# Optimization experiments

Measured on AMD Instinct MI355X. Metric: run time of the kernel, lower is better.

Reference implementation:

```python
import jax, jax.numpy as jnp
import numpy as np

B, L, D, E, H, FFN_MULT = 16, 2048, 512, 8, 8, 4
HD = D // H
ALPHA, BETA, LN_EPS = 1.0, 0.5, 1e-5


def _ln(x, g, b):
    mu = x.mean(-1, keepdims=True)
    var = ((x - mu) ** 2).mean(-1, keepdims=True)
    return (x - mu) * jax.lax.rsqrt(var + LN_EPS) * g + b


def setup_inputs() -> dict:
    key = jax.random.key(0)
    ks = jax.random.split(key, 20)
    s = 0.02
    return {
        "query": jax.random.normal(ks[0], (B, D), jnp.float32),
        "retrieved": jax.random.normal(ks[1], (B, L, D), jnp.float32),
        "w_gate": jax.random.normal(ks[2], (D, E), jnp.float32) * s,
        "ln_q_g": jnp.ones((E, D), jnp.float32),
        "ln_q_b": jnp.zeros((E, D), jnp.float32),
        "Wq": jax.random.normal(ks[3], (E, D, D), jnp.float32) * s,
        "bq": jnp.zeros((E, D), jnp.float32),
        "Wk": jax.random.normal(ks[4], (E, D, D), jnp.float32) * s,
        "bk": jnp.zeros((E, D), jnp.float32),
        "Wv": jax.random.normal(ks[5], (E, D, D), jnp.float32) * s,
        "bv": jnp.zeros((E, D), jnp.float32),
        "Wo": jax.random.normal(ks[6], (E, D, D), jnp.float32) * s,
        "bo": jnp.zeros((E, D), jnp.float32),
        "ln_o_g": jnp.ones((E, D), jnp.float32),
        "ln_o_b": jnp.zeros((E, D), jnp.float32),
        "W1": jax.random.normal(ks[7], (E, D, FFN_MULT * D), jnp.float32) * s,
        "b1": jnp.zeros((E, FFN_MULT * D), jnp.float32),
        "W2": jax.random.normal(ks[8], (E, FFN_MULT * D, D), jnp.float32) * s,
        "b2": jnpp_zeros((E, D)) if False else jnp.zeros((E, D), jnp.float32),
    }


def reference(query, retrieved, w_gate, ln_q_g, ln_q_b, Wq, bq, Wk, bk, Wv, bv,
              Wo, bo, ln_o_g, ln_o_b, W1, b1, W2, b2):
    # Gating (eval mode: no noise, r=None) -> (B, E)
    gates = jax.nn.softmax(query @ w_gate, axis=-1)

    # Per-expert LayerNorm of the (shared) query: normalize once, affine per expert
    mu = query.mean(-1, keepdims=True)
    var = ((query - mu) ** 2).mean(-1, keepdims=True)
    xn = (query - mu) * jax.lax.rsqrt(var + LN_EPS)              # (B, D)
    qn = xn[:, None, :] * ln_q_g[None] + ln_q_b[None]            # (B, E, D)

    # Cross-attention, query length 1, per expert (MHA with in/out proj)
    qh = (jnp.einsum('bed,edk->bek', qn, Wq) + bq).reshape(B, E, H, HD)
    k = (jnp.einsum('bld,edk->belk', retrieved, Wk) + bk[:, None, :]).reshape(B, E, L, H, HD)
    v = (jnp.einsum('bld,edk->belk', retrieved, Wv) + bv[:, None, :]).reshape(B, E, L, H, HD)
    scores = jnp.einsum('behc,belhc->behl', qh, k) / jnp.sqrt(jnp.float32(HD))
    probs = jax.nn.softmax(scores, axis=-1)                      # (B, E, H, L)
    attn = jnp.einsum('behl,belhc->behc', probs, v).reshape(B, E, D)
    attn_out = jnp.einsum('bed,edk->bek', attn, Wo) + bo         # (B, E, D)
    avg_probs = probs.mean(axis=2)                               # (B, E, L) heads averaged

    # Residual + FFN (dropouts inactive at eval)
    x = query[:, None, :] + attn_out                             # (B, E, D)
    xo = _ln(x, ln_o_g[None], ln_o_b[None])
    h = jax.nn.gelu(jnp.einsum('bed,edf->bef', xo, W1) + b1, approximate=False)
    y = jnp.einsum('bef,efd->bed', h, W2) + b2 + x               # expert_outs (B, E, D)

    # Entropy-derived reliability
    p = jnp.clip(avg_probs, 1e-12, None)
    Hent = -(p * jnp.log(p)).sum(-1)                             # (B, E)
    s_all = jnp.exp(-BETA * Hent)

    gt = gates * s_all
    gt = gt / (gt.sum(-1, keepdims=True) + 1e-9)
    mixture = (gt[..., None] * y).sum(1)                         # (B, D)
    fused = ALPHA * mixture + (1.0 - ALPHA) * query
    return fused, y, gt
```

## Files before the change

### kernel.cpp

```cpp
#include <hip/hip_runtime.h>
#include <math.h>

#define CB 16
#define CL 2048
#define CD 512
#define CE 8
#define CH 8
#define CEH 64
#define CF 2048

typedef __bf16 bf16x8 __attribute__((ext_vector_type(8)));
typedef float f32x4 __attribute__((ext_vector_type(4)));

#define GLL16(srcp, dstp) __builtin_amdgcn_global_load_lds( \
    (const __attribute__((address_space(1))) unsigned int*)(srcp), \
    (__attribute__((address_space(3))) unsigned int*)(dstp), 16, 0, 0)

#define WS_GATES 0
#define WS_XN    (WS_GATES + CB*CE)
#define WS_QN    (WS_XN + CB*CD)
#define WS_QH    (WS_QN + CB*CE*CD)
#define WS_SBIAS (WS_QH + CB*CE*CD)
#define WS_WK    (WS_SBIAS + CB*CE*CH)
#define WS_SC    (WS_WK + CB*CEH*CD)
#define WS_PART  WS_SC
#define WS_PART1 (WS_PART + 524288)
#define WS_RMAX  (WS_SC + CB*CL*CEH)
#define WS_RINV  (WS_RMAX + CB*CEH)
#define WS_ENT   (WS_RINV + CB*CEH)
#define WS_ATTN  (WS_ENT + CB*CE*8)
#define WS_X     (WS_ATTN + CB*CE*CD)
#define WS_XO    (WS_X + CB*CE*CD)
#define WS_HB    (WS_XO + CB*CE*CD)
#define WS_RP    (WS_HB + CB*CE*CF)
#define WS_PB16  (WS_RP + 8*CB*CEH*CD)

__global__ __launch_bounds__(256) void k1_gates_qn(
    const float* __restrict__ q, const float* __restrict__ wg,
    const float* __restrict__ g, const float* __restrict__ bln,
    float* __restrict__ qn, float* __restrict__ gates) {
  int b = blockIdx.x, t = threadIdx.x;
  __shared__ float red[256];
  __shared__ float logits[CE];
  float v0 = q[b*CD + t], v1 = q[b*CD + 256 + t];
  red[t] = v0 + v1; __syncthreads();
  for (int s = 128; s > 0; s >>= 1) { if (t < s) red[t] += red[t+s]; __syncthreads(); }
  float mu = red[0] * (1.0f/CD); __syncthreads();
  float c0 = v0 - mu, c1 = v1 - mu;
  red[t] = c0*c0 + c1*c1; __syncthreads();
  for (int s = 128; s > 0; s >>= 1) { if (t < s) red[t] += red[t+s]; __syncthreads(); }
  float rstd = rsqrtf(red[0] * (1.0f/CD) + 1e-5f); __syncthreads();
  float xn0 = c0 * rstd, xn1 = c1 * rstd;
  #pragma unroll
  for (int e = 0; e < CE; e++) {
    qn[(b*CE + e)*CD + t]       = xn0 * g[e*CD + t]       + bln[e*CD + t];
    qn[(b*CE + e)*CD + 256 + t] = xn1 * g[e*CD + 256 + t] + bln[e*CD + 256 + t];
  }
  float ge[CE];
  #pragma unroll
  for (int e = 0; e < CE; e++) ge[e] = v0 * wg[t*CE + e] + v1 * wg[(256+t)*CE + e];
  for (int e = 0; e < CE; e++) {
    red[t] = ge[e]; __syncthreads();
    for (int s = 128; s > 0; s >>= 1) { if (t < s) red[t] += red[t+s]; __syncthreads(); }
    if (t == 0) logits[e] = red[0];
    __syncthreads();
  }
  if (t == 0) {
    float m = logits[0];
    for (int e = 1; e < CE; e++) m = fmaxf(m, logits[e]);
    float s = 0.f, ex[CE];
    for (int e = 0; e < CE; e++) { ex[e] = __expf(logits[e] - m); s += ex[e]; }
    for (int e = 0; e < CE; e++) gates[b*CE + e] = ex[e] / s;
  }
}

template<int KC>
__global__ __launch_bounds__(256) void gstream(
    const float* __restrict__ X, int xb_, int xe_,
    const float* __restrict__ W, size_t we_, int ldw,
    float* __restrict__ P, int ntiles, size_t pc_, int pb_, int pe_) {
  int e = blockIdx.y;
  int nt = blockIdx.x % ntiles, kc = blockIdx.x / ntiles;
  int n0 = nt * 64, k0 = kc * KC;
  __shared__ float xs[KC][16];
  __shared__ float red[16][64];
  int t = threadIdx.x;
  for (int idx = t; idx < KC * 16; idx += 256) {
    int k = idx >> 4, b = idx & 15;
    xs[k][b] = X[(size_t)b * xb_ + (size_t)e * xe_ + k0 + k];
  }
  __syncthreads();
  int n = t & 63, kq = t >> 6;
  float acc[16] = {};
  const float* Wp = W + (size_t)e * we_ + (size_t)k0 * ldw + n0 + n;
  #pragma unroll 4
  for (int k = kq * (KC/4); k < (kq+1) * (KC/4); k++) {
    float w = Wp[(size_t)k * ldw];
    const float4* xp = reinterpret_cast<const float4*>(xs[k]);
    float4 x0 = xp[0], x1 = xp[1], x2 = xp[2], x3 = xp[3];
    acc[0]  += x0.x*w; acc[1]  += x0.y*w; acc[2]  += x0.z*w; acc[3]  += x0.w*w;
    acc[4]  += x1.x*w; acc[5]  += x1.y*w; acc[6]  += x1.z*w; acc[7]  += x1.w*w;
    acc[8]  += x2.x*w; acc[9]  += x2.y*w; acc[10] += x2.z*w; acc[11] += x2.w*w;
    acc[12] += x3.x*w; acc[13] += x3.y*w; acc[14] += x3.z*w; acc[15] += x3.w*w;
  }
  if (kq == 0) {
    #pragma unroll
    for (int b = 0; b < 16; b++) red[b][n] = acc[b];
  }
  __syncthreads();
  #pragma unroll
  for (int qq = 1; qq < 4; qq++) {
    if (kq == qq) {
      #pragma unroll
      for (int b = 0; b < 16; b++) red[b][n] += acc[b];
    }
    __syncthreads();
  }
  #pragma unroll
  for (int i = 0; i < 4; i++) {
    int b = kq*4 + i;
    P[(size_t)kc*pc_ + (size_t)b*pb_ + (size_t)e*pe_ + n0 + n] = red[b][n];
  }
}

__global__ __launch_bounds__(256) void gstream_v(
    const float* __restrict__ rp, const float* __restrict__ Wv,
    float* __restrict__ P) {
  int eh = blockIdx.y, kc = blockIdx.x;
  int e = eh >> 3, h = eh & 7;
  int k0 = kc * 64;
  __shared__ float xs[64][20];
  __shared__ float red[16][64];
  int t = threadIdx.x;
  for (int idx = t; idx < 64 * 16; idx += 256) {
    int k = idx & 63, b = idx >> 6;
    float s = 0.f;
    #pragma unroll
    for (int c = 0; c < 8; c++)
      s += rp[(size_t)c*(CB*CEH*CD) + ((size_t)(b*CEH + eh))*CD + k0 + k];
    xs[k][b] = s;
  }
  __syncthreads();
  int n = t & 63, kq = t >> 6;
  float acc[16] = {};
  const float* Wp = Wv + (size_t)e*CD*CD + (size_t)k0*CD + h*64 + n;
  #pragma unroll 4
  for (int k = kq*16; k < kq*16 + 16; k++) {
    float w = Wp[(size_t)k * CD];
    const float4* xp = reinterpret_cast<const float4*>(&xs[k][0]);
    float4 x0 = xp[0], x1 = xp[1], x2 = xp[2], x3 = xp[3];
    acc[0]  += x0.x*w; acc[1]  += x0.y*w; acc[2]  += x0.z*w; acc[3]  += x0.w*w;
    acc[4]  += x1.x*w; acc[5]  += x1.y*w; acc[6]  += x1.z*w; acc[7]  += x1.w*w;
    acc[8]  += x2.x*w; acc[9]  += x2.y*w; acc[10] += x2.z*w; acc[11] += x2.w*w;
    acc[12] += x3.x*w; acc[13] += x3.y*w; acc[14] += x3.z*w; acc[15] += x3.w*w;
  }
  if (kq == 0) { 
    #pragma unroll
    for (int b = 0; b < 16; b++) red[b][n] = acc[b]; }
  __syncthreads();
  #pragma unroll
  for (int qq = 1; qq < 4; qq++) {
    if (kq == qq) {
      #pragma unroll
      for (int b = 0; b < 16; b++) red[b][n] += acc[b];
    }
    __syncthreads();
  }
  #pragma unroll
  for (int i = 0; i < 4; i++) {
    int b = kq*4 + i;
    P[(size_t)kc*65536 + (size_t)b*4096 + (size_t)eh*64 + n] = red[b][n];
  }
}

__global__ __launch_bounds__(256) void gstream_wo(
    const float* __restrict__ Pv, const float* __restrict__ bv,
    const float* __restrict__ Wo, float* __restrict__ P) {
  int e = blockIdx.y;
  int nt = blockIdx.x % 8, kc = blockIdx.x / 8;
  int n0 = nt * 64, k0 = kc * 64;
  __shared__ float xs[64][20];
  __shared__ float red[16][64];
  int t = threadIdx.x;
  for (int idx = t; idx < 64 * 16; idx += 256) {
    int k = idx & 63, b = idx >> 6;
    float s = bv[e*CD + k0 + k];
    #pragma unroll
    for (int c = 0; c < 8; c++)
      s += Pv[(size_t)c*65536 + (size_t)b*4096 + e*512 + k0 + k];
    xs[k][b] = s;
  }
  __syncthreads();
  int n = t & 63, kq = t >> 6;
  float acc[16] = {};
  const float* Wp = Wo + (size_t)e*CD*CD + (size_t)k0*CD + n0 + n;
  #pragma unroll 4
  for (int k = kq*16; k < kq*16 + 16; k++) {
    float w = Wp[(size_t)k * CD];
    const float4* xp = reinterpret_cast<const float4*>(&xs[k][0]);
    float4 x0 = xp[0], x1 = xp[1], x2 = xp[2], x3 = xp[3];
    acc[0]  += x0.x*w; acc[1]  += x0.y*w; acc[2]  += x0.z*w; acc[3]  += x0.w*w;
    acc[4]  += x1.x*w; acc[5]  += x1.y*w; acc[6]  += x1.z*w; acc[7]  += x1.w*w;
    acc[8]  += x2.x*w; acc[9]  += x2.y*w; acc[10] += x2.z*w; acc[11] += x2.w*w;
    acc[12] += x3.x*w; acc[13] += x3.y*w; acc[14] += x3.z*w; acc[15] += x3.w*w;
  }
  if (kq == 0) {
    #pragma unroll
    for (int b = 0; b < 16; b++) red[b][n] = acc[b]; }
  __syncthreads();
  #pragma unroll
  for (int qq = 1; qq < 4; qq++) {
    if (kq == qq) {
      #pragma unroll
      for (int b = 0; b < 16; b++) red[b][n] += acc[b];
    }
    __syncthreads();
  }
  #pragma unroll
  for (int i = 0; i < 4; i++) {
    int b = kq*4 + i;
    P[(size_t)kc*65536 + (size_t)b*4096 + (size_t)e*512 + n0 + n] = red[b][n];
  }
}

__global__ __launch_bounds__(512) void comb_qh_sbias(
    const float* __restrict__ P, const float* __restrict__ bq,
    const float* __restrict__ bk, float* __restrict__ qh,
    float* __restrict__ sbias) {
  int be = blockIdx.x, b = be >> 3, e = be & 7, t = threadIdx.x;
  float s = bq[e*CD + t];
  #pragma unroll
  for (int c = 0; c < 8; c++)
    s += P[(size_t)c*65536 + (size_t)b*4096 + e*512 + t];
  qh[be*CD + t] = s;
  float w = s * bk[e*CD + t];
  #pragma unroll
  for (int off = 32; off > 0; off >>= 1) w += __shfl_down(w, off);
  if ((t & 63) == 0) sbias[be*CH + (t >> 6)] = w;
}

__global__ __launch_bounds__(512) void comb_o_lno(
    const float* __restrict__ P, const float* __restrict__ bo,
    const float* __restrict__ q, const float* __restrict__ g,
    const float* __restrict__ bb, float* __restrict__ xb,
    float* __restrict__ xo) {
  int be = blockIdx.x, b = be >> 3, e = be & 7, t = threadIdx.x;
  float v = q[b*CD + t] + bo[e*CD + t];
  #pragma unroll
  for (int c = 0; c < 8; c++)
    v += P[(size_t)c*65536 + (size_t)b*4096 + e*512 + t];
  xb[be*CD + t] = v;
  __shared__ float red[512];
  red[t] = v; __syncthreads();
  for (int s = 256; s > 0; s >>= 1) { if (t < s) red[t] += red[t+s]; __syncthreads(); }
  float mu = red[0] * (1.0f/CD); __syncthreads();
  float c0 = v - mu;
  red[t] = c0*c0; __syncthreads();
  for (int s = 256; s > 0; s >>= 1) { if (t < s) red[t] += red[t+s]; __syncthreads(); }
  float rstd = rsqrtf(red[0] * (1.0f/CD) + 1e-5f);
  xo[be*CD + t] = c0*rstd*g[e*CD + t] + bb[e*CD + t];
}

__global__ __launch_bounds__(256) void comb4_gelu(
    const float* __restrict__ P, const float* __restrict__ bias,
    float* __restrict__ out) {
  int i = blockIdx.x*256 + threadIdx.x;
  float s = bias[i & 16383];
  #pragma unroll
  for (int c = 0; c < 4; c++) s += P[(size_t)c*262144 + i];
  out[i] = 0.5f*s*(1.f + erff(s*0.70710678118f));
}

__global__ __launch_bounds__(512) void comb_ffn2_final(
    const float* __restrict__ P, const float* __restrict__ b2,
    const float* __restrict__ xb, const float* __restrict__ gates,
    const float* __restrict__ entp, float* __restrict__ yout,
    float* __restrict__ fused, float* __restrict__ gtout) {
  int b = blockIdx.x, t = threadIdx.x;
  __shared__ float gt_s[CE];
  if (t < CE) {
    float Hs = 0.f;
    #pragma unroll
    for (int c = 0; c < 8; c++) Hs += entp[(b*CE + t)*8 + c];
    gt_s[t] = gates[b*CE + t] * __expf(-0.5f * Hs);
  }
  __syncthreads();
  if (t == 0) {
    float s = 0.f;
    for (int e = 0; e < CE; e++) s += gt_s[e];
    s += 1e-9f;
    for (int e = 0; e < CE; e++) gt_s[e] /= s;
  }
  __syncthreads();
  float acc = 0.f;
  #pragma unroll
  for (int e = 0; e < CE; e++) {
    float y = b2[e*CD + t] + xb[(b*CE + e)*CD + t];
    #pragma unroll
    for (int c = 0; c < 8; c++)
      y += P[(size_t)c*65536 + (size_t)b*4096 + e*512 + t];
    yout[(b*CE + e)*CD + t] = y;
    acc += gt_s[e] * y;
  }
  fused[b*CD + t] = acc;
  if (t < CE) gtout[b*CE + t] = gt_s[t];
}

__global__ __launch_bounds__(256) void k4_wkeff(
    const float* __restrict__ Wk, const float* __restrict__ qh,
    __bf16* __restrict__ wkh) {
  int e = blockIdx.y;
  int h = blockIdx.x >> 3, dt = blockIdx.x & 7;
  int d0 = dt * 64;
  __shared__ float wks[64][65];
  __shared__ float qs[64][16];
  __shared__ float red[16][64];
  int t = threadIdx.x;
  for (int idx = t; idx < 64*64; idx += 256) {
    int c = idx & 63, d = idx >> 6;
    wks[c][d] = Wk[(size_t)e*CD*CD + (size_t)(d0+d)*CD + h*64 + c];
  }
  for (int idx = t; idx < 64*16; idx += 256) {
    int c = idx >> 4, b = idx & 15;
    qs[c][b] = qh[(b*CE + e)*CD + h*64 + c];
  }
  __syncthreads();
  int d = t & 63, cq = t >> 6;
  float acc[16] = {};
  #pragma unroll 4
  for (int c = cq*16; c < cq*16 + 16; c++) {
    float w = wks[c][d];
    const float4* xp = reinterpret_cast<const float4*>(qs[c]);
    float4 x0 = xp[0], x1 = xp[1], x2 = xp[2], x3 = xp[3];
    acc[0]  += x0.x*w; acc[1]  += x0.y*w; acc[2]  += x0.z*w; acc[3]  += x0.w*w;
    acc[4]  += x1.x*w; acc[5]  += x1.y*w; acc[6]  += x1.z*w; acc[7]  += x1.w*w;
    acc[8]  += x2.x*w; acc[9]  += x2.y*w; acc[10] += x2.z*w; acc[11] += x2.w*w;
    acc[12] += x3.x*w; acc[13] += x3.y*w; acc[14] += x3.z*w; acc[15] += x3.w*w;
  }
  if (cq == 0) { 
    #pragma unroll
    for (int b = 0; b < 16; b++) red[b][d] = acc[b]; }
  __syncthreads();
  #pragma unroll
  for (int qq = 1; qq < 4; qq++) {
    if (cq == qq) {
      #pragma unroll
      for (int b = 0; b < 16; b++) red[b][d] += acc[b];
    }
    __syncthreads();
  }
  int eh = e*8 + h;
  #pragma unroll
  for (int i = 0; i < 4; i++) {
    int b = cq*4 + i;
    wkh[((size_t)(b*CEH + eh))*CD + d0 + d] = (__bf16)red[b][d];
  }
}

__global__ __launch_bounds__(256) void k5_mfma(
    const float* __restrict__ ret, const __bf16* __restrict__ wkh,
    const float* __restrict__ sbias, float* __restrict__ sc,
    float* __restrict__ lmax, float* __restrict__ lsum) {
  int b = blockIdx.y, lt = blockIdx.x, t = threadIdx.x;
  int w = t >> 6, lane = t & 63;
  int lnlo = lane & 15, lnhi = lane >> 4;
  int lh = w & 1, ehh = w >> 1;
  int l0blk = lt*32;
  int ehbase = ehh*32;
  __shared__ __align__(16) char ldsbuf[32768];
  f32x4 acc[2];
  acc[0] = (f32x4){0.f,0.f,0.f,0.f};
  acc[1] = (f32x4){0.f,0.f,0.f,0.f};
  const float*  retb  = ret + (size_t)(b*CL + l0blk)*CD;
  const __bf16* wkhb  = wkh + (size_t)b*CEH*CD;

  int rs0 = t,        rl0 = rs0 >> 4, rg0 = ((rs0 & 15) ^ (rl0 & 15)) << 2;
  int rs1 = t + 256,  rl1 = rs1 >> 4, rg1 = ((rs1 & 15) ^ (rl1 & 15)) << 2;
  int ws0 = t,        we0 = ws0 >> 3, wg0 = ((ws0 & 7) ^ (we0 & 7)) << 3;
  int ws1 = t + 256,  we1 = ws1 >> 3, wg1 = ((ws1 & 7) ^ (we1 & 7)) << 3;

  #define K5_STAGE(bufi, kt) do {                                          \
    char* rB = ldsbuf + (bufi)*8192;                                       \
    char* wB = ldsbuf + 16384 + (bufi)*8192;                               \
    int dofs = (kt)*64;                                                    \
    GLL16(retb + (size_t)rl0*CD + dofs + rg0, rB + rs0*16);                \
    GLL16(retb + (size_t)rl1*CD + dofs + rg1, rB + rs1*16);                \
    GLL16(wkhb + (size_t)we0*CD + dofs + wg0, wB + ws0*16);                \
    GLL16(wkhb + (size_t)we1*CD + dofs + wg1, wB + ws1*16);                \
  } while (0)

  K5_STAGE(0, 0);
  __syncthreads();
  #pragma unroll
  for (int kt = 0; kt < 8; kt++) {
    int cur = kt & 1;
    if (kt < 7) K5_STAGE(cur ^ 1, kt + 1);
    const char* rB = ldsbuf + cur*8192;
    const char* wB = ldsbuf + 16384 + cur*8192;
    #pragma unroll
    for (int sub = 0; sub < 2; sub++) {
      int g0 = (sub*8 + lnhi*2 + 0) ^ lnlo;
      int g1 = (sub*8 + lnhi*2 + 1) ^ lnlo;
      float4 f0 = *reinterpret_cast<const float4*>(rB + (lh*16 + lnlo)*256 + g0*16);
      float4 f1 = *reinterpret_cast<const float4*>(rB + (lh*16 + lnlo)*256 + g1*16);
      bf16x8 bfrag;
      bfrag[0]=(__bf16)f0.x; bfrag[1]=(__bf16)f0.y; bfrag[2]=(__bf16)f0.z; bfrag[3]=(__bf16)f0.w;
      bfrag[4]=(__bf16)f1.x; bfrag[5]=(__bf16)f1.y; bfrag[6]=(__bf16)f1.z; bfrag[7]=(__bf16)f1.w;
      int ga = (sub*4 + lnhi) ^ (lnlo & 7);
      bf16x8 a0 = *reinterpret_cast<const bf16x8*>(wB + (ehbase + 0*16 + lnlo)*128 + ga*16);
      bf16x8 a1 = *reinterpret_cast<const bf16x8*>(wB + (ehbase + 1*16 + lnlo)*128 + ga*16);
      acc[0] = __builtin_amdgcn_mfma_f32_16x16x32_bf16(a0, bfrag, acc[0], 0, 0, 0);
      acc[1] = __builtin_amdgcn_mfma_f32_16x16x32_bf16(a1, bfrag, acc[1], 0, 0, 0);
    }
    __syncthreads();
  }
  #undef K5_STAGE

  int strip = lt*2 + lh;
  int l = l0blk + lh*16 + lnlo;
  #pragma unroll
  for (int et = 0; et < 2; et++) {
    #pragma unroll
    for (int i = 0; i < 4; i++) {
      int eh = ehbase + et*16 + lnhi*4 + i;
      float v = acc[et][i]*0.125f + sbias[b*CEH + eh]*0.125f;
      sc[((size_t)(b*CEH + eh))*CL + l] = v;
      float m = v;
      m = fmaxf(m, __shfl_xor(m, 1));
      m = fmaxf(m, __shfl_xor(m, 2));
      m = fmaxf(m, __shfl_xor(m, 4));
      m = fmaxf(m, __shfl_xor(m, 8));
      float s = __expf(v - m);
      s += __shfl_xor(s, 1);
      s += __shfl_xor(s, 2);
      s += __shfl_xor(s, 4);
      s += __shfl_xor(s, 8);
      if (lnlo == et*4 + i) {
        lmax[((size_t)(b*CEH + eh))*128 + strip] = m;
        lsum[((size_t)(b*CEH + eh))*128 + strip] = s;
      }
    }
  }
}

__global__ __launch_bounds__(256) void k5b2(
    const float* __restrict__ lmax, const float* __restrict__ lsum,
    float* __restrict__ rmax, float* __restrict__ rinv) {
  int b = blockIdx.x, t = threadIdx.x, eh = t & 63, q = t >> 6;
  const float* lm = lmax + ((size_t)(b*CEH + eh))*128 + q*32;
  const float* ls = lsum + ((size_t)(b*CEH + eh))*128 + q*32;
  float M = -1e30f, S = 0.f;
  for (int i = 0; i < 32; i++) {
    float m2 = lm[i], s2 = ls[i];
    float Mn = fmaxf(M, m2);
    S = S*__expf(M - Mn) + s2*__expf(m2 - Mn);
    M = Mn;
  }
  __shared__ float sm[4][64], ss[4][64];
  sm[q][eh] = M; ss[q][eh] = S;
  __syncthreads();
  if (q == 0) {
    #pragma unroll
    for (int i = 1; i < 4; i++) {
      float m2 = sm[i][eh], s2 = ss[i][eh];
      float Mn = fmaxf(M, m2);
      S = S*__expf(M - Mn) + s2*__expf(m2 - Mn);
      M = Mn;
    }
    rmax[b*CEH + eh] = M;
    rinv[b*CEH + eh] = 1.f / S;
  }
}

__global__ __launch_bounds__(256) void k5n(
    const float* __restrict__ sc, const float* __restrict__ rmax,
    const float* __restrict__ rinv, __bf16* __restrict__ pb,
    float* __restrict__ entp) {
  int e = blockIdx.x, b = blockIdx.y, lc = blockIdx.z, t = threadIdx.x;
  int l = lc*256 + t;
  float pbav = 0.f;
  #pragma unroll
  for (int h = 0; h < 8; h++) {
    size_t ix = ((size_t)(b*CEH + e*8 + h))*CL + l;
    float p = __expf(sc[ix] - rmax[b*CEH + e*8 + h]) * rinv[b*CEH + e*8 + h];
    pb[ix] = (__bf16)p;
    pbav += p;
  }
  pbav = fmaxf(pbav*0.125f, 1e-12f);
  float ent = -pbav * __logf(pbav);
  __shared__ float red[256];
  red[t] = ent; __syncthreads();
  for (int s = 128; s > 0; s >>= 1) { if (t < s) red[t] += red[t+s]; __syncthreads(); }
  if (t == 0) entp[(b*CE + e)*8 + lc] = red[0];
}

__global__ __launch_bounds__(256) void k6_mfma(
    const __bf16* __restrict__ pb, const float* __restrict__ ret,
    float* __restrict__ part) {
  int b = blockIdx.y;
  int dt = blockIdx.x & 7, lc = blockIdx.x >> 3;
  int d0 = dt*64, l0 = lc*256;
  int t = threadIdx.x, w = t >> 6, lane = t & 63;
  int lnlo = lane & 15, lnhi = lane >> 4;
  __shared__ __bf16 Bs[2][64][40];
  f32x4 acc[4];
  #pragma unroll
  for (int et = 0; et < 4; et++) acc[et] = (f32x4){0.f,0.f,0.f,0.f};
  const __bf16* pbb = pb + ((size_t)(b*CEH) + lnlo)*CL + l0 + lnhi*8;
  int srow = t & 31, scol = (t >> 5)*8;
  const float* retb = ret + ((size_t)(b*CL) + l0 + srow)*CD + d0 + scol;
  float4 v0 = *reinterpret_cast<const float4*>(retb);
  float4 v1 = *reinterpret_cast<const float4*>(retb + 4);
  bf16x8 ap0 = *reinterpret_cast<const bf16x8*>(pbb);
  bf16x8 ap1 = *reinterpret_cast<const bf16x8*>(pbb + (size_t)16*CL);
  bf16x8 ap2 = *reinterpret_cast<const bf16x8*>(pbb + (size_t)32*CL);
  bf16x8 ap3 = *reinterpret_cast<const bf16x8*>(pbb + (size_t)48*CL);
  #pragma unroll
  for (int kt = 0; kt < 8; kt++) {
    int cur = kt & 1;
    Bs[cur][scol+0][srow] = (__bf16)v0.x; Bs[cur][scol+1][srow] = (__bf16)v0.y;
    Bs[cur][scol+2][srow] = (__bf16)v0.z; Bs[cur][scol+3][srow] = (__bf16)v0.w;
    Bs[cur][scol+4][srow] = (__bf16)v1.x; Bs[cur][scol+5][srow] = (__bf16)v1.y;
    Bs[cur][scol+6][srow] = (__bf16)v1.z; Bs[cur][scol+7][srow] = (__bf16)v1.w;
    bf16x8 an0, an1, an2, an3;
    if (kt < 7) {
      v0 = *reinterpret_cast<const float4*>(retb + (size_t)(kt+1)*32*CD);
      v1 = *reinterpret_cast<const float4*>(retb + (size_t)(kt+1)*32*CD + 4);
      an0 = *reinterpret_cast<const bf16x8*>(pbb + (kt+1)*32);
      an1 = *reinterpret_cast<const bf16x8*>(pbb + (size_t)16*CL + (kt+1)*32);
      an2 = *reinterpret_cast<const bf16x8*>(pbb + (size_t)32*CL + (kt+1)*32);
      an3 = *reinterpret_cast<const bf16x8*>(pbb + (size_t)48*CL + (kt+1)*32);
    }
    __syncthreads();
    bf16x8 bfrag = *reinterpret_cast<const bf16x8*>(&Bs[cur][w*16 + lnlo][lnhi*8]);
    acc[0] = __builtin_amdgcn_mfma_f32_16x16x32_bf16(ap0, bfrag, acc[0], 0, 0, 0);
    acc[1] = __builtin_amdgcn_mfma_f32_16x16x32_bf16(ap1, bfrag, acc[1], 0, 0, 0);
    acc[2] = __builtin_amdgcn_mfma_f32_16x16x32_bf16(ap2, bfrag, acc[2], 0, 0, 0);
    acc[3] = __builtin_amdgcn_mfma_f32_16x16x32_bf16(ap3, bfrag, acc[3], 0, 0, 0);
    if (kt < 7) { ap0 = an0; ap1 = an1; ap2 = an2; ap3 = an3; }
  }
  float* dst = part + (size_t)lc*(CB*CEH*CD);
  int d = d0 + w*16 + lnlo;
  #pragma unroll
  for (int et = 0; et < 4; et++) {
    #pragma unroll
    for (int i = 0; i < 4; i++) {
      int eh = et*16 + lnhi*4 + i;
      dst[((size_t)(b*CEH + eh))*CD + d] = acc[et][i];
    }
  }
}

extern "C" void kernel_launch(void* const* d_in, const int* in_sizes, int n_in,
                              void* d_out, int out_size, void* d_ws, size_t ws_size,
                              hipStream_t stream) {
  const float* q    = (const float*)d_in[0];
  const float* ret  = (const float*)d_in[1];
  const float* wg   = (const float*)d_in[2];
  const float* lnqg = (const float*)d_in[3];
  const float* lnqb = (const float*)d_in[4];
  const float* Wq   = (const float*)d_in[5];
  const float* bq   = (const float*)d_in[6];
  const float* Wk   = (const float*)d_in[7];
  const float* bk   = (const float*)d_in[8];
  const float* Wv   = (const float*)d_in[9];
  const float* bv   = (const float*)d_in[10];
  const float* Wo   = (const float*)d_in[11];
  const float* bo   = (const float*)d_in[12];
  const float* lnog = (const float*)d_in[13];
  const float* lnob = (const float*)d_in[14];
  const float* W1   = (const float*)d_in[15];
  const float* b1   = (const float*)d_in[16];
  const float* W2   = (const float*)d_in[17];
  const float* b2   = (const float*)d_in[18];

  float* ws = (float*)d_ws;
  float* fused = (float*)d_out;
  float* yout  = fused + CB*CD;
  float* gtout = yout + CB*CE*CD;

  float* gates = ws + WS_GATES;
  float* qn    = ws + WS_QN;
  float* qh    = ws + WS_QH;
  float* sbias = ws + WS_SBIAS;
  __bf16* wkh  = (__bf16*)(ws + WS_WK);
  float* sc    = ws + WS_SC;
  float* part0 = ws + WS_PART;
  float* part1 = ws + WS_PART1;
  float* rmax  = ws + WS_RMAX;
  float* rinv  = ws + WS_RINV;
  float* entp  = ws + WS_ENT;
  float* xb    = ws + WS_X;
  float* xo    = ws + WS_XO;
  float* hbuf  = ws + WS_HB;
  float* rpart = ws + WS_RP;
  __bf16* pb16 = (__bf16*)(ws + WS_PB16);
  float* lmax  = rpart;
  float* lsum  = rpart + CB*CEH*128;

  k1_gates_qn<<<CB, 256, 0, stream>>>(q, wg, lnqg, lnqb, qn, gates);
  gstream<64><<<dim3(64, CE), 256, 0, stream>>>(qn, CE*CD, CD, Wq, (size_t)CD*CD, CD,
                                                part0, 8, 65536, CE*CD, CD);
  comb_qh_sbias<<<CB*CE, 512, 0, stream>>>(part0, bq, bk, qh, sbias);
  k4_wkeff<<<dim3(64, CE), 256, 0, stream>>>(Wk, qh, wkh);
  k5_mfma<<<dim3(64, CB), 256, 0, stream>>>(ret, wkh, sbias, sc, lmax, lsum);
  k5b2<<<CB, 256, 0, stream>>>(lmax, lsum, rmax, rinv);
  k5n<<<dim3(CE, CB, 8), 256, 0, stream>>>(sc, rmax, rinv, pb16, entp);
  k6_mfma<<<dim3(64, CB), 256, 0, stream>>>(pb16, ret, rpart);
  gstream_v<<<dim3(8, CEH), 256, 0, stream>>>(rpart, Wv, part1);
  gstream_wo<<<dim3(64, CE), 256, 0, stream>>>(part1, bv, Wo, part0);
  comb_o_lno<<<CB*CE, 512, 0, stream>>>(part0, bo, q, lnog, lnob, xb, xo);
  gstream<128><<<dim3(128, CE), 256, 0, stream>>>(xo, CE*CD, CD, W1, (size_t)CD*CF, CF,
                                                  part0, 32, 262144, CE*CF, CF);
  comb4_gelu<<<1024, 256, 0, stream>>>(part0, b1, hbuf);
  gstream<256><<<dim3(64, CE), 256, 0, stream>>>(hbuf, CE*CF, CF, W2, (size_t)CF*CD, CD,
                                                 part0, 8, 65536, CE*CD, CD);
  comb_ffn2_final<<<CB, 512, 0, stream>>>(part0, b2, xb, gates, entp, yout, fused, gtout);
}
```

Before: 129.0 us.

## Fuse combine kernels into consumers and use wave shuffles in gating

Folds three small combine kernels into the kernels that consume their results: the Q-projection partial sum and sbias go into k4_wkeff, the softmax max/sum reduction goes into k5n, and the bias+GELU step goes into a new W2 streaming kernel. This cuts three launches and the round trips through qh, rmax/rinv and hbuf. In exchange the fused kernels recompute the combines redundantly across blocks (for example GELU is recomputed per n-tile, and the lmax/lsum merge per l-chunk). The gating kernel also replaces shared-memory tree reductions with wave shuffles and fewer barriers.

```diff
diff --git a/kernel.cpp b/kernel.cpp
--- a/kernel.cpp
+++ b/kernel.cpp
@@ -25,9 +25,7 @@
 #define WS_SC    (WS_WK + CB*CEH*CD)
 #define WS_PART  WS_SC
 #define WS_PART1 (WS_PART + 524288)
-#define WS_RMAX  (WS_SC + CB*CL*CEH)
-#define WS_RINV  (WS_RMAX + CB*CEH)
-#define WS_ENT   (WS_RINV + CB*CEH)
+#define WS_ENT   (WS_SC + CB*CL*CEH)
 #define WS_ATTN  (WS_ENT + CB*CE*8)
 #define WS_X     (WS_ATTN + CB*CE*CD)
 #define WS_XO    (WS_X + CB*CE*CD)
@@ -40,37 +38,54 @@
     const float* __restrict__ g, const float* __restrict__ bln,
     float* __restrict__ qn, float* __restrict__ gates) {
   int b = blockIdx.x, t = threadIdx.x;
-  __shared__ float red[256];
-  __shared__ float logits[CE];
+  int w = t >> 6, lane = t & 63;
+  __shared__ float r1[4], r2[4];
+  __shared__ float gp[4][8];
   float v0 = q[b*CD + t], v1 = q[b*CD + 256 + t];
-  red[t] = v0 + v1; __syncthreads();
-  for (int s = 128; s > 0; s >>= 1) { if (t < s) red[t] += red[t+s]; __syncthreads(); }
-  float mu = red[0] * (1.0f/CD); __syncthreads();
+  float s = v0 + v1;
+  #pragma unroll
+  for (int m = 32; m >= 1; m >>= 1) s += __shfl_xor(s, m);
+  if (lane == 0) r1[w] = s;
+  __syncthreads();
+  float mu = (r1[0]+r1[1]+r1[2]+r1[3]) * (1.0f/CD);
   float c0 = v0 - mu, c1 = v1 - mu;
-  red[t] = c0*c0 + c1*c1; __syncthreads();
-  for (int s = 128; s > 0; s >>= 1) { if (t < s) red[t] += red[t+s]; __syncthreads(); }
-  float rstd = rsqrtf(red[0] * (1.0f/CD) + 1e-5f); __syncthreads();
+  s = c0*c0 + c1*c1;
+  #pragma unroll
+  for (int m = 32; m >= 1; m >>= 1) s += __shfl_xor(s, m);
+  if (lane == 0) r2[w] = s;
+  float ge[CE];
+  #pragma unroll
+  for (int e = 0; e < CE; e++) ge[e] = v0 * wg[t*CE + e] + v1 * wg[(256+t)*CE + e];
+  #pragma unroll
+  for (int m = 32; m >= 1; m >>= 1) {
+    #pragma unroll
+    for (int e = 0; e < CE; e++) ge[e] += __shfl_xor(ge[e], m);
+  }
+  if (lane == 0) {
+    #pragma unroll
+    for (int e = 0; e < CE; e++) gp[w][e] = ge[e];
+  }
+  __syncthreads();
+  float rstd = rsqrtf((r2[0]+r2[1]+r2[2]+r2[3]) * (1.0f/CD) + 1e-5f);
   float xn0 = c0 * rstd, xn1 = c1 * rstd;
   #pragma unroll
   for (int e = 0; e < CE; e++) {
     qn[(b*CE + e)*CD + t]       = xn0 * g[e*CD + t]       + bln[e*CD + t];
     qn[(b*CE + e)*CD + 256 + t] = xn1 * g[e*CD + 256 + t] + bln[e*CD + 256 + t];
   }
-  float ge[CE];
-  #pragma unroll
-  for (int e = 0; e < CE; e++) ge[e] = v0 * wg[t*CE + e] + v1 * wg[(256+t)*CE + e];
-  for (int e = 0; e < CE; e++) {
-    red[t] = ge[e]; __syncthreads();
-    for (int s = 128; s > 0; s >>= 1) { if (t < s) red[t] += red[t+s]; __syncthreads(); }
-    if (t == 0) logits[e] = red[0];
-    __syncthreads();
-  }
   if (t == 0) {
-    float m = logits[0];
-    for (int e = 1; e < CE; e++) m = fmaxf(m, logits[e]);
-    float s = 0.f, ex[CE];
-    for (int e = 0; e < CE; e++) { ex[e] = __expf(logits[e] - m); s += ex[e]; }
-    for (int e = 0; e < CE; e++) gates[b*CE + e] = ex[e] / s;
+    float logit[CE];
+    float m = -1e30f;
+    #pragma unroll
+    for (int e = 0; e < CE; e++) {
+      logit[e] = gp[0][e] + gp[1][e] + gp[2][e] + gp[3][e];
+      m = fmaxf(m, logit[e]);
+    }
+    float ssum = 0.f, ex[CE];
+    #pragma unroll
+    for (int e = 0; e < CE; e++) { ex[e] = __expf(logit[e] - m); ssum += ex[e]; }
+    #pragma unroll
+    for (int e = 0; e < CE; e++) gates[b*CE + e] = ex[e] / ssum;
   }
 }
 
@@ -223,20 +238,54 @@
   }
 }
 
-__global__ __launch_bounds__(512) void comb_qh_sbias(
-    const float* __restrict__ P, const float* __restrict__ bq,
-    const float* __restrict__ bk, float* __restrict__ qh,
-    float* __restrict__ sbias) {
-  int be = blockIdx.x, b = be >> 3, e = be & 7, t = threadIdx.x;
-  float s = bq[e*CD + t];
-  #pragma unroll
-  for (int c = 0; c < 8; c++)
-    s += P[(size_t)c*65536 + (size_t)b*4096 + e*512 + t];
-  qh[be*CD + t] = s;
-  float w = s * bk[e*CD + t];
-  #pragma unroll
-  for (int off = 32; off > 0; off >>= 1) w += __shfl_down(w, off);
-  if ((t & 63) == 0) sbias[be*CH + (t >> 6)] = w;
+__global__ __launch_bounds__(256) void gstream_w2(
+    const float* __restrict__ P1, const float* __restrict__ b1,
+    const float* __restrict__ W2, float* __restrict__ Pout) {
+  int e = blockIdx.y;
+  int nt = blockIdx.x % 8, kc = blockIdx.x / 8;
+  int n0 = nt * 64, k0 = kc * 256;
+  __shared__ float xs[256][16];
+  __shared__ float red[16][64];
+  int t = threadIdx.x;
+  for (int idx = t; idx < 256 * 16; idx += 256) {
+    int k = idx >> 4, b = idx & 15;
+    float v = b1[e*CF + k0 + k];
+    #pragma unroll
+    for (int c = 0; c < 4; c++)
+      v += P1[(size_t)c*262144 + (size_t)b*16384 + e*2048 + k0 + k];
+    xs[k][b] = 0.5f*v*(1.f + erff(v*0.70710678118f));
+  }
+  __syncthreads();
+  int n = t & 63, kq = t >> 6;
+  float acc[16] = {};
+  const float* Wp = W2 + (size_t)e*CF*CD + (size_t)k0*CD + n0 + n;
+  #pragma unroll 4
+  for (int k = kq*64; k < kq*64 + 64; k++) {
+    float w = Wp[(size_t)k * CD];
+    const float4* xp = reinterpret_cast<const float4*>(xs[k]);
+    float4 x0 = xp[0], x1 = xp[1], x2 = xp[2], x3 = xp[3];
+    acc[0]  += x0.x*w; acc[1]  += x0.y*w; acc[2]  += x0.z*w; acc[3]  += x0.w*w;
+    acc[4]  += x1.x*w; acc[5]  += x1.y*w; acc[6]  += x1.z*w; acc[7]  += x1.w*w;
+    acc[8]  += x2.x*w; acc[9]  += x2.y*w; acc[10] += x2.z*w; acc[11] += x2.w*w;
+    acc[12] += x3.x*w; acc[13] += x3.y*w; acc[14] += x3.z*w; acc[15] += x3.w*w;
+  }
+  if (kq == 0) {
+    #pragma unroll
+    for (int b = 0; b < 16; b++) red[b][n] = acc[b]; }
+  __syncthreads();
+  #pragma unroll
+  for (int qq = 1; qq < 4; qq++) {
+    if (kq == qq) {
+      #pragma unroll
+      for (int b = 0; b < 16; b++) red[b][n] += acc[b];
+    }
+    __syncthreads();
+  }
+  #pragma unroll
+  for (int i = 0; i < 4; i++) {
+    int b = kq*4 + i;
+    Pout[(size_t)kc*65536 + (size_t)b*4096 + (size_t)e*512 + n0 + n] = red[b][n];
+  }
 }
 
 __global__ __launch_bounds__(512) void comb_o_lno(
@@ -261,16 +310,6 @@
   xo[be*CD + t] = c0*rstd*g[e*CD + t] + bb[e*CD + t];
 }
 
-__global__ __launch_bounds__(256) void comb4_gelu(
-    const float* __restrict__ P, const float* __restrict__ bias,
-    float* __restrict__ out) {
-  int i = blockIdx.x*256 + threadIdx.x;
-  float s = bias[i & 16383];
-  #pragma unroll
-  for (int c = 0; c < 4; c++) s += P[(size_t)c*262144 + i];
-  out[i] = 0.5f*s*(1.f + erff(s*0.70710678118f));
-}
-
 __global__ __launch_bounds__(512) void comb_ffn2_final(
     const float* __restrict__ P, const float* __restrict__ b2,
     const float* __restrict__ xb, const float* __restrict__ gates,
@@ -307,8 +346,9 @@
 }
 
 __global__ __launch_bounds__(256) void k4_wkeff(
-    const float* __restrict__ Wk, const float* __restrict__ qh,
-    __bf16* __restrict__ wkh) {
+    const float* __restrict__ Wk, const float* __restrict__ Pq,
+    const float* __restrict__ bq, const float* __restrict__ bk,
+    __bf16* __restrict__ wkh, float* __restrict__ sbias) {
   int e = blockIdx.y;
   int h = blockIdx.x >> 3, dt = blockIdx.x & 7;
   int d0 = dt * 64;
@@ -322,9 +362,25 @@
   }
   for (int idx = t; idx < 64*16; idx += 256) {
     int c = idx >> 4, b = idx & 15;
-    qs[c][b] = qh[(b*CE + e)*CD + h*64 + c];
-  }
-  __syncthreads();
+    float s = bq[e*CD + h*64 + c];
+    #pragma unroll
+    for (int cc = 0; cc < 8; cc++)
+      s += Pq[(size_t)cc*65536 + (size_t)b*4096 + e*512 + h*64 + c];
+    qs[c][b] = s;
+  }
+  __syncthreads();
+  if (dt == 0) {
+    int bb = t >> 4, ii = t & 15;
+    float p = 0.f;
+    #pragma unroll
+    for (int j = 0; j < 4; j++)
+      p += qs[ii*4 + j][bb] * bk[e*CD + h*64 + ii*4 + j];
+    p += __shfl_xor(p, 1);
+    p += __shfl_xor(p, 2);
+    p += __shfl_xor(p, 4);
+    p += __shfl_xor(p, 8);
+    if (ii == 0) sbias[bb*CEH + e*8 + h] = p;
+  }
   int d = t & 63, cq = t >> 6;
   float acc[16] = {};
   #pragma unroll 4
@@ -443,46 +499,41 @@
   }
 }
 
-__global__ __launch_bounds__(256) void k5b2(
-    const float* __restrict__ lmax, const float* __restrict__ lsum,
-    float* __restrict__ rmax, float* __restrict__ rinv) {
-  int b = blockIdx.x, t = threadIdx.x, eh = t & 63, q = t >> 6;
-  const float* lm = lmax + ((size_t)(b*CEH + eh))*128 + q*32;
-  const float* ls = lsum + ((size_t)(b*CEH + eh))*128 + q*32;
-  float M = -1e30f, S = 0.f;
-  for (int i = 0; i < 32; i++) {
-    float m2 = lm[i], s2 = ls[i];
-    float Mn = fmaxf(M, m2);
-    S = S*__expf(M - Mn) + s2*__expf(m2 - Mn);
-    M = Mn;
-  }
-  __shared__ float sm[4][64], ss[4][64];
-  sm[q][eh] = M; ss[q][eh] = S;
-  __syncthreads();
-  if (q == 0) {
-    #pragma unroll
-    for (int i = 1; i < 4; i++) {
-      float m2 = sm[i][eh], s2 = ss[i][eh];
+__global__ __launch_bounds__(256) void k5n(
+    const float* __restrict__ sc, const float* __restrict__ lmax,
+    const float* __restrict__ lsum, __bf16* __restrict__ pb,
+    float* __restrict__ entp) {
+  int e = blockIdx.x, b = blockIdx.y, lc = blockIdx.z, t = threadIdx.x;
+  __shared__ float M_s[8], I_s[8];
+  {
+    int g = t >> 5, lane = t & 31;
+    int eh = e*8 + g;
+    const float* lm = lmax + ((size_t)(b*CEH + eh))*128;
+    const float* ls = lsum + ((size_t)(b*CEH + eh))*128;
+    float M = -1e30f, S = 0.f;
+    #pragma unroll
+    for (int j = 0; j < 4; j++) {
+      float m2 = lm[lane + j*32], s2 = ls[lane + j*32];
       float Mn = fmaxf(M, m2);
       S = S*__expf(M - Mn) + s2*__expf(m2 - Mn);
       M = Mn;
     }
-    rmax[b*CEH + eh] = M;
-    rinv[b*CEH + eh] = 1.f / S;
-  }
-}
-
-__global__ __launch_bounds__(256) void k5n(
-    const float* __restrict__ sc, const float* __restrict__ rmax,
-    const float* __restrict__ rinv, __bf16* __restrict__ pb,
-    float* __restrict__ entp) {
-  int e = blockIdx.x, b = blockIdx.y, lc = blockIdx.z, t = threadIdx.x;
+    #pragma unroll
+    for (int mask = 16; mask >= 1; mask >>= 1) {
+      float Mo = __shfl_xor(M, mask), So = __shfl_xor(S, mask);
+      float Mn = fmaxf(M, Mo);
+      S = S*__expf(M - Mn) + So*__expf(Mo - Mn);
+      M = Mn;
+    }
+    if (lane == 0) { M_s[g] = M; I_s[g] = 1.f / S; }
+  }
+  __syncthreads();
   int l = lc*256 + t;
   float pbav = 0.f;
   #pragma unroll
   for (int h = 0; h < 8; h++) {
     size_t ix = ((size_t)(b*CEH + e*8 + h))*CL + l;
-    float p = __expf(sc[ix] - rmax[b*CEH + e*8 + h]) * rinv[b*CEH + e*8 + h];
+    float p = __expf(sc[ix] - M_s[h]) * I_s[h];
     pb[ix] = (__bf16)p;
     pbav += p;
   }
@@ -581,18 +632,14 @@
 
   float* gates = ws + WS_GATES;
   float* qn    = ws + WS_QN;
-  float* qh    = ws + WS_QH;
   float* sbias = ws + WS_SBIAS;
   __bf16* wkh  = (__bf16*)(ws + WS_WK);
   float* sc    = ws + WS_SC;
   float* part0 = ws + WS_PART;
   float* part1 = ws + WS_PART1;
-  float* rmax  = ws + WS_RMAX;
-  float* rinv  = ws + WS_RINV;
   float* entp  = ws + WS_ENT;
   float* xb    = ws + WS_X;
   float* xo    = ws + WS_XO;
-  float* hbuf  = ws + WS_HB;
   float* rpart = ws + WS_RP;
   __bf16* pb16 = (__bf16*)(ws + WS_PB16);
   float* lmax  = rpart;
@@ -601,19 +648,15 @@
   k1_gates_qn<<<CB, 256, 0, stream>>>(q, wg, lnqg, lnqb, qn, gates);
   gstream<64><<<dim3(64, CE), 256, 0, stream>>>(qn, CE*CD, CD, Wq, (size_t)CD*CD, CD,
                                                 part0, 8, 65536, CE*CD, CD);
-  comb_qh_sbias<<<CB*CE, 512, 0, stream>>>(part0, bq, bk, qh, sbias);
-  k4_wkeff<<<dim3(64, CE), 256, 0, stream>>>(Wk, qh, wkh);
+  k4_wkeff<<<dim3(64, CE), 256, 0, stream>>>(Wk, part0, bq, bk, wkh, sbias);
   k5_mfma<<<dim3(64, CB), 256, 0, stream>>>(ret, wkh, sbias, sc, lmax, lsum);
-  k5b2<<<CB, 256, 0, stream>>>(lmax, lsum, rmax, rinv);
-  k5n<<<dim3(CE, CB, 8), 256, 0, stream>>>(sc, rmax, rinv, pb16, entp);
+  k5n<<<dim3(CE, CB, 8), 256, 0, stream>>>(sc, lmax, lsum, pb16, entp);
   k6_mfma<<<dim3(64, CB), 256, 0, stream>>>(pb16, ret, rpart);
   gstream_v<<<dim3(8, CEH), 256, 0, stream>>>(rpart, Wv, part1);
   gstream_wo<<<dim3(64, CE), 256, 0, stream>>>(part1, bv, Wo, part0);
   comb_o_lno<<<CB*CE, 512, 0, stream>>>(part0, bo, q, lnog, lnob, xb, xo);
   gstream<128><<<dim3(128, CE), 256, 0, stream>>>(xo, CE*CD, CD, W1, (size_t)CD*CF, CF,
                                                   part0, 32, 262144, CE*CF, CF);
-  comb4_gelu<<<1024, 256, 0, stream>>>(part0, b1, hbuf);
-  gstream<256><<<dim3(64, CE), 256, 0, stream>>>(hbuf, CE*CF, CF, W2, (size_t)CF*CD, CD,
-                                                 part0, 8, 65536, CE*CD, CD);
-  comb_ffn2_final<<<CB, 512, 0, stream>>>(part0, b2, xb, gates, entp, yout, fused, gtout);
-}
+  gstream_w2<<<dim3(64, CE), 256, 0, stream>>>(part0, b1, W2, rpart);
+  comb_ffn2_final<<<CB, 512, 0, stream>>>(rpart, b2, xb, gates, entp, yout, fused, gtout);
+}
```

Result: slower. 133.6 us (+3.5%).
